# Kernel tuning notes

Hardware: AMD Instinct MI355X
Metric: run time of the kernel (lower is better)

## Reference

```python
import jax, jax.numpy as jnp
import numpy as np

NUM_HEADS = 12

def setup_inputs() -> dict:
    key = jax.random.key(0)
    k1, k2, k3, k4 = jax.random.split(key, 4)
    B, N, D = 8, 1024, 768
    x = jax.random.normal(k1, (B, N, D), dtype=jnp.float32)
    mask = jax.random.randint(k2, (B, N), 0, 2, dtype=jnp.int32)
    Wqkv = jax.random.normal(k3, (3 * D, D), dtype=jnp.float32) * (D ** -0.5)
    Wproj = jax.random.normal(k4, (D, D), dtype=jnp.float32) * (D ** -0.5)
    bproj = jnp.zeros((D,), dtype=jnp.float32)
    return {"x": x, "mask": mask, "Wqkv": Wqkv, "Wproj": Wproj, "bproj": bproj}

def reference(x, mask, Wqkv, Wproj, bproj):
    B, N, D = x.shape
    H = NUM_HEADS
    hd = D // H
    scale = hd ** -0.5
    # QKV projection (no bias), split into q,k,v of shape [B,H,N,hd]
    qkv = jnp.einsum('bnd,ed->bne', x, Wqkv).reshape(B, N, 3, H, hd)
    qkv = jnp.transpose(qkv, (2, 0, 3, 1, 4))
    q, k, v = qkv[0], qkv[1], qkv[2]
    # padding mask: attend where both query and key are valid; masked-out
    # (padded) query rows attend only to themselves (diagonal) to avoid NaNs
    m = mask.astype(bool)  # [B,N]
    pair = m[:, None, :, None] & m[:, None, None, :]          # [B,1,N,N]
    diag = jnp.eye(N, dtype=bool)[None, None]                 # [1,1,N,N]
    attn_mask = pair | (diag & ~m[:, None, :, None])          # [B,1,N,N]
    scores = jnp.einsum('bhnd,bhmd->bhnm', q, k) * scale      # [B,H,N,N]
    scores = jnp.where(attn_mask, scores, jnp.finfo(scores.dtype).min)
    attn = jax.nn.softmax(scores, axis=-1)
    out = jnp.einsum('bhnm,bhmd->bhnd', attn, v)
    out = jnp.transpose(out, (0, 2, 1, 3)).reshape(B, N, D)
    out = jnp.einsum('bnd,ed->bne', out, Wproj) + bproj
    return out
```

## Files before the change

### kernel.cpp

```cpp
#include <hip/hip_runtime.h>
#include <hip/hip_bf16.h>
#include <stdint.h>


typedef unsigned short u16;
typedef unsigned int u32;
typedef __attribute__((ext_vector_type(8))) short short8;
typedef __attribute__((ext_vector_type(4))) float f32x4;

#define MFMA16(a, b, c) __builtin_amdgcn_mfma_f32_16x16x32_bf16((a), (b), (c), 0, 0, 0)

static __device__ __forceinline__ u16 f2bf(float f) {
    __hip_bfloat16 h = __float2bfloat16(f);
    return *(u16*)&h;
}
static __device__ __forceinline__ void gld16(const u16* g, u16* l) {
  __builtin_amdgcn_global_load_lds(
      (const __attribute__((address_space(1))) void*)g,
      (__attribute__((address_space(3))) void*)l, 16, 0, 0);
}

__global__ __launch_bounds__(256) void cvt_bf16(
    const float* __restrict__ s0, u16* __restrict__ d0, int n0,
    const float* __restrict__ s1, u16* __restrict__ d1, int n1,
    const float* __restrict__ s2, u16* __restrict__ d2, int n2) {
  int i = (blockIdx.x * 256 + threadIdx.x) * 4;
  const float* s; u16* d;
  if (i < n0) { s = s0 + i; d = d0 + i; }
  else if ((i -= n0) < n1) { s = s1 + i; d = d1 + i; }
  else if ((i -= n1) < n2) { s = s2 + i; d = d2 + i; }
  else return;
  float4 v = *(const float4*)s;
  ushort4 o;
  o.x = f2bf(v.x); o.y = f2bf(v.y); o.z = f2bf(v.z); o.w = f2bf(v.w);
  *(ushort4*)d = o;
}

__global__ __launch_bounds__(512, 4) void gemm_qkv_p32(
    const u16* __restrict__ A,
    const u16* __restrict__ B,
    u16* __restrict__ C) {
  constexpr int K = 768, LDC = 2304, NTIL = K / 32;
  __shared__ u16 lds[2][(256 + 128) * 32];
  const int tid = threadIdx.x;
  const int w = tid >> 6, l = tid & 63;
  const int lane16 = l & 15, quad = l >> 4;
  const int wr = w >> 2, wc = w & 3;

  const int orig = blockIdx.x;
  const int logical = (orig & 7) * 72 + (orig >> 3);
  const int i0 = (logical / 18) * 256, j0 = (logical % 18) * 128;

  f32x4 acc[8][2];
  #pragma unroll
  for (int m = 0; m < 8; m++)
    #pragma unroll
    for (int n = 0; n < 2; n++) acc[m][n] = (f32x4){0.f, 0.f, 0.f, 0.f};

  auto stage = [&](int buf, int t) {
    const int k0 = t * 32;
    u16* Ad = &lds[buf][0];
    #pragma unroll
    for (int s = 0; s < 2; s++) {
      int lin = tid + s * 512;
      int row = lin >> 2, j = lin & 3;
      gld16(&A[(size_t)(i0 + row) * K + k0 + ((j ^ ((row >> 1) & 3)) * 8)], &Ad[lin * 8]);
    }
    {
      u16* Bd = &lds[buf][256 * 32];
      int row = tid >> 2, j = tid & 3;
      gld16(&B[(size_t)(j0 + row) * K + k0 + ((j ^ ((row >> 1) & 3)) * 8)], &Bd[tid * 8]);
    }
  };

  stage(0, 0);
  stage(1, 1);
  asm volatile("s_waitcnt vmcnt(3)" ::: "memory");
  __builtin_amdgcn_s_barrier();

  for (int t = 0; t < NTIL; t++) {
    const u16* Al = &lds[t & 1][0];
    const u16* Bl = &lds[t & 1][256 * 32];
    short8 bf[2], af[8];
    #pragma unroll
    for (int n = 0; n < 2; n++) {
      int row = wc * 32 + n * 16 + lane16;
      int ch = quad ^ ((row >> 1) & 3);
      bf[n] = *(const short8*)&Bl[row * 32 + ch * 8];
    }
    #pragma unroll
    for (int mi = 0; mi < 8; mi++) {
      int row = wr * 128 + mi * 16 + lane16;
      int ch = quad ^ ((row >> 1) & 3);
      af[mi] = *(const short8*)&Al[row * 32 + ch * 8];
    }
    asm volatile("s_waitcnt lgkmcnt(0)" ::: "memory");
    __builtin_amdgcn_sched_barrier(0);
    __builtin_amdgcn_s_barrier();
    if (t + 2 < NTIL) stage(t & 1, t + 2);
    __builtin_amdgcn_s_setprio(1);
    #pragma unroll
    for (int mi = 0; mi < 8; mi++)
      #pragma unroll
      for (int n = 0; n < 2; n++)
        acc[mi][n] = MFMA16(af[mi], bf[n], acc[mi][n]);
    __builtin_amdgcn_s_setprio(0);
    if (t + 2 < NTIL) asm volatile("s_waitcnt vmcnt(3)" ::: "memory");
    else              asm volatile("s_waitcnt vmcnt(0)" ::: "memory");
    __builtin_amdgcn_s_barrier();
  }

  #pragma unroll
  for (int m = 0; m < 8; m++) {
    #pragma unroll
    for (int n = 0; n < 2; n++) {
      int col = j0 + wc * 32 + n * 16 + lane16;
      #pragma unroll
      for (int r = 0; r < 4; r++) {
        int row = i0 + wr * 128 + m * 16 + quad * 4 + r;
        C[(size_t)row * LDC + col] = f2bf(acc[m][n][r]);
      }
    }
  }
}

__global__ __launch_bounds__(256, 3) void gemm_proj_p32(
    const u16* __restrict__ A,
    const u16* __restrict__ B,
    float* __restrict__ C,
    const float* __restrict__ bias) {
  constexpr int K = 768, LDC = 768, NTIL = K / 32;
  __shared__ u16 lds[2][(128 + 64) * 32];
  const int tid = threadIdx.x;
  const int w = tid >> 6, l = tid & 63;
  const int lane16 = l & 15, quad = l >> 4;
  const int mh = (w & 1) * 64;
  const int nh = (w >> 1) * 32;

  const int orig = blockIdx.x;
  const int logical = (orig & 7) * 96 + (orig >> 3);
  const int i0 = (logical / 12) * 128, j0 = (logical % 12) * 64;

  f32x4 acc[4][2];
  #pragma unroll
  for (int m = 0; m < 4; m++)
    #pragma unroll
    for (int n = 0; n < 2; n++) acc[m][n] = (f32x4){0.f, 0.f, 0.f, 0.f};

  auto stage = [&](int buf, int t) {
    const int k0 = t * 32;
    u16* Ad = &lds[buf][0];
    #pragma unroll
    for (int s = 0; s < 2; s++) {
      int lin = tid + s * 256;
      int row = lin >> 2, j = lin & 3;
      gld16(&A[(size_t)(i0 + row) * K + k0 + ((j ^ ((row >> 1) & 3)) * 8)], &Ad[lin * 8]);
    }
    {
      u16* Bd = &lds[buf][128 * 32];
      int row = tid >> 2, j = tid & 3;
      gld16(&B[(size_t)(j0 + row) * K + k0 + ((j ^ ((row >> 1) & 3)) * 8)], &Bd[tid * 8]);
    }
  };

  stage(0, 0);
  stage(1, 1);
  asm volatile("s_waitcnt vmcnt(3)" ::: "memory");
  __builtin_amdgcn_s_barrier();

  for (int t = 0; t < NTIL; t++) {
    const u16* Al = &lds[t & 1][0];
    const u16* Bl = &lds[t & 1][128 * 32];
    short8 bf[2];
    #pragma unroll
    for (int n = 0; n < 2; n++) {
      int row = nh + n * 16 + lane16;
      int ch = quad ^ ((row >> 1) & 3);
      bf[n] = *(const short8*)&Bl[row * 32 + ch * 8];
    }
    #pragma unroll
    for (int p = 0; p < 2; p++) {
      short8 af[2];
      #pragma unroll
      for (int mi = 0; mi < 2; mi++) {
        int row = mh + (2 * p + mi) * 16 + lane16;
        int ch = quad ^ ((row >> 1) & 3);
        af[mi] = *(const short8*)&Al[row * 32 + ch * 8];
      }
      if (p == 1) {
        asm volatile("s_waitcnt lgkmcnt(0)" ::: "memory");
        __builtin_amdgcn_sched_barrier(0);
        __builtin_amdgcn_s_barrier();
        if (t + 2 < NTIL) stage(t & 1, t + 2);
      }
      __builtin_amdgcn_s_setprio(1);
      #pragma unroll
      for (int mi = 0; mi < 2; mi++)
        #pragma unroll
        for (int n = 0; n < 2; n++)
          acc[2 * p + mi][n] = MFMA16(af[mi], bf[n], acc[2 * p + mi][n]);
      __builtin_amdgcn_s_setprio(0);
    }
    if (t + 2 < NTIL) asm volatile("s_waitcnt vmcnt(3)" ::: "memory");
    else              asm volatile("s_waitcnt vmcnt(0)" ::: "memory");
    __builtin_amdgcn_s_barrier();
  }

  #pragma unroll
  for (int m = 0; m < 4; m++) {
    #pragma unroll
    for (int n = 0; n < 2; n++) {
      int col = j0 + nh + n * 16 + lane16;
      #pragma unroll
      for (int r = 0; r < 4; r++) {
        int row = i0 + mh + m * 16 + quad * 4 + r;
        C[(size_t)row * LDC + col] = acc[m][n][r] + bias[col];
      }
    }
  }
}

__global__ __launch_bounds__(256, 3) void attn_mfma(
    const u16* __restrict__ qkv,
    const int* __restrict__ mask,
    u16* __restrict__ ctx) {
  __shared__ u16 Ks[64][72];
  __shared__ u16 Vt[64][72];
  __shared__ u16 Ps[4][32][72];
  __shared__ float mkb_all[1024];

  const int tid = threadIdx.x;
  const int w = tid >> 6, l = tid & 63;
  const int lane16 = l & 15, quad = l >> 4;
  const int idx = blockIdx.x;
  const int bh = idx % 96;
  const int rb = idx / 96;
  const int b = bh / 12, h = bh % 12;
  const int n0 = rb * 128;
  const int baseRow = b * 1024;

  const float K1 = 0.18033688011112043f;
  const float K0 = -23.083120654223415f;

  const int key_s = tid >> 2, ds_s = (tid & 3) * 16;
  const int kA_s = (tid & 31) * 2, dg_s = tid >> 5;

  {
    int4 mv = *(const int4*)&mask[baseRow + tid * 4];
    f32x4 mf;
    mf[0] = mv.x ? K0 : -1e38f;
    mf[1] = mv.y ? K0 : -1e38f;
    mf[2] = mv.z ? K0 : -1e38f;
    mf[3] = mv.w ? K0 : -1e38f;
    *(f32x4*)&mkb_all[tid * 4] = mf;
  }

  short8 qfrag[2][2];
  #pragma unroll
  for (int qt = 0; qt < 2; qt++) {
    const u16* qp = qkv + (size_t)(baseRow + n0 + w*32 + qt*16 + lane16) * 2304 + h*64;
    #pragma unroll
    for (int ks = 0; ks < 2; ks++)
      qfrag[qt][ks] = *(const short8*)(qp + ks*32 + quad*8);
  }

  f32x4 oacc[2][4];
  #pragma unroll
  for (int qt = 0; qt < 2; qt++)
    #pragma unroll
    for (int nt = 0; nt < 4; nt++) oacc[qt][nt] = (f32x4){0.f, 0.f, 0.f, 0.f};
  f32x4 lsum4[2] = {(f32x4){0.f,0.f,0.f,0.f}, (f32x4){0.f,0.f,0.f,0.f}};

  uint4 kr0, kr1, vr0, vr1;
  {
    const u16* kp = qkv + (size_t)(baseRow + key_s) * 2304 + 768 + h*64 + ds_s;
    kr0 = *(const uint4*)kp;
    kr1 = *(const uint4*)(kp + 8);
    const u16* vp = qkv + (size_t)(baseRow + kA_s) * 2304 + 1536 + h*64 + dg_s*8;
    vr0 = *(const uint4*)vp;
    vr1 = *(const uint4*)(vp + 2304);
  }

  for (int c = 0; c < 16; c++) {
    if (c) __syncthreads();

    *(uint4*)&Ks[key_s][ds_s]     = kr0;
    *(uint4*)&Ks[key_s][ds_s + 8] = kr1;
    {
      const u16* va = (const u16*)&vr0;
      const u16* vb = (const u16*)&vr1;
      #pragma unroll
      for (int j = 0; j < 8; j++)
        *(unsigned int*)&Vt[dg_s*8 + j][kA_s] =
            (unsigned int)va[j] | ((unsigned int)vb[j] << 16);
    }

    if (c + 1 < 16) {
      const u16* kp = qkv + (size_t)(baseRow + (c+1)*64 + key_s) * 2304 + 768 + h*64 + ds_s;
      kr0 = *(const uint4*)kp;
      kr1 = *(const uint4*)(kp + 8);
      const u16* vp = qkv + (size_t)(baseRow + (c+1)*64 + kA_s) * 2304 + 1536 + h*64 + dg_s*8;
      vr0 = *(const uint4*)vp;
      vr1 = *(const uint4*)(vp + 2304);
    }
    __syncthreads();

    f32x4 sacc[4][2];
    #pragma unroll
    for (int kt = 0; kt < 4; kt++)
      #pragma unroll
      for (int qt = 0; qt < 2; qt++) sacc[kt][qt] = (f32x4){0.f, 0.f, 0.f, 0.f};
    #pragma unroll
    for (int ks = 0; ks < 2; ks++) {
      short8 kf[4];
      #pragma unroll
      for (int kt = 0; kt < 4; kt++)
        kf[kt] = *(const short8*)&Ks[kt*16 + lane16][ks*32 + quad*8];
      __builtin_amdgcn_s_setprio(1);
      #pragma unroll
      for (int kt = 0; kt < 4; kt++)
        #pragma unroll
        for (int qt = 0; qt < 2; qt++)
          sacc[kt][qt] = MFMA16(kf[kt], qfrag[qt][ks], sacc[kt][qt]);
      __builtin_amdgcn_s_setprio(0);
    }

    #pragma unroll
    for (int kt = 0; kt < 4; kt++) {
      f32x4 mk4 = *(const f32x4*)&mkb_all[c*64 + kt*16 + quad*4];
      #pragma unroll
      for (int qt = 0; qt < 2; qt++) {
        float e0 = __builtin_amdgcn_exp2f(fmaf(sacc[kt][qt][0], K1, mk4[0]));
        float e1 = __builtin_amdgcn_exp2f(fmaf(sacc[kt][qt][1], K1, mk4[1]));
        float e2 = __builtin_amdgcn_exp2f(fmaf(sacc[kt][qt][2], K1, mk4[2]));
        float e3 = __builtin_amdgcn_exp2f(fmaf(sacc[kt][qt][3], K1, mk4[3]));
        lsum4[qt][0] += e0; lsum4[qt][1] += e1;
        lsum4[qt][2] += e2; lsum4[qt][3] += e3;
        uint2 pv;
        asm("v_cvt_pk_bf16_f32 %0, %1, %2" : "=v"(pv.x) : "v"(e0), "v"(e1));
        asm("v_cvt_pk_bf16_f32 %0, %1, %2" : "=v"(pv.y) : "v"(e2), "v"(e3));
        *(uint2*)&Ps[w][qt*16 + lane16][kt*16 + quad*4] = pv;
      }
    }

    #pragma unroll
    for (int kc = 0; kc < 2; kc++) {
      short8 pf[2], vf[4];
      #pragma unroll
      for (int qt = 0; qt < 2; qt++)
        pf[qt] = *(const short8*)&Ps[w][qt*16 + lane16][kc*32 + quad*8];
      #pragma unroll
      for (int nt = 0; nt < 4; nt++)
        vf[nt] = *(const short8*)&Vt[nt*16 + lane16][kc*32 + quad*8];
      __builtin_amdgcn_s_setprio(1);
      #pragma unroll
      for (int qt = 0; qt < 2; qt++)
        #pragma unroll
        for (int nt = 0; nt < 4; nt++)
          oacc[qt][nt] = MFMA16(pf[qt], vf[nt], oacc[qt][nt]);
      __builtin_amdgcn_s_setprio(0);
    }
  }

  float linv[2][4];
  #pragma unroll
  for (int qt = 0; qt < 2; qt++) {
    float s = lsum4[qt][0] + lsum4[qt][1] + lsum4[qt][2] + lsum4[qt][3];
    s += __shfl_xor(s, 16);
    s += __shfl_xor(s, 32);
    #pragma unroll
    for (int r = 0; r < 4; r++)
      linv[qt][r] = 1.0f / __shfl(s, quad*4 + r);
  }
  #pragma unroll
  for (int qt = 0; qt < 2; qt++) {
    #pragma unroll
    for (int r = 0; r < 4; r++) {
      int rl = w*32 + qt*16 + quad*4 + r;
      int rg = n0 + rl;
      int mq = (mkb_all[n0 + rl] != -1e38f);
      #pragma unroll
      for (int nt = 0; nt < 4; nt++) {
        u16 outv;
        if (mq) {
          outv = f2bf(oacc[qt][nt][r] * linv[qt][r]);
        } else {
          outv = qkv[(size_t)(baseRow + rg) * 2304 + 1536 + h*64 + nt*16 + lane16];
        }
        ctx[(size_t)(baseRow + rg) * 768 + h*64 + nt*16 + lane16] = outv;
      }
    }
  }
}

extern "C" void kernel_launch(void* const* d_in, const int* in_sizes, int n_in,
                              void* d_out, int out_size, void* d_ws, size_t ws_size,
                              hipStream_t stream) {
  const float* x     = (const float*)d_in[0];
  const int*   mask  = (const int*)d_in[1];
  const float* Wqkv  = (const float*)d_in[2];
  const float* Wproj = (const float*)d_in[3];
  const float* bproj = (const float*)d_in[4];
  float* out = (float*)d_out;

  const int NX = 8192 * 768;
  const int NQ = 2304 * 768;
  const int NP = 768 * 768;

  char* wsb = (char*)d_ws;
  u16* qkv    = (u16*)wsb;
  u16* ctx    = (u16*)(wsb + (size_t)8192 * 2304 * 2);
  u16* xb     = (u16*)(wsb + (size_t)8192 * 2304 * 2 + (size_t)8192 * 768 * 2);
  u16* wqkvb  = xb + NX;
  u16* wprojb = wqkvb + NQ;

  int cvt_blocks = ((NX + NQ + NP) / 4 + 255) / 256;
  cvt_bf16<<<dim3(cvt_blocks), 256, 0, stream>>>(x, xb, NX, Wqkv, wqkvb, NQ, Wproj, wprojb, NP);

  gemm_qkv_p32<<<dim3(576), 512, 0, stream>>>(xb, wqkvb, qkv);
  attn_mfma<<<dim3(768), 256, 0, stream>>>(qkv, mask, ctx);
  gemm_proj_p32<<<dim3(768), 256, 0, stream>>>(ctx, wprojb, out, bproj);
}
```

Measured before the change: 183.5 us.

## Double-buffer K/V LDS tiles and apply XOR swizzle instead of padding

Replaces the padded LDS arrays for K, transposed V and P with unpadded 64-column arrays that use an XOR swizzle on 8-element chunks, to avoid bank conflicts on the MFMA fragment reads and writes. K and V tiles become double-buffered by chunk parity, which removes the barrier at the top of each iteration and lets the next tile's stores overlap the previous tile's reads. LDS use grows for K/V but shrinks for padding, so occupancy at 3 blocks per CU may shift. The narrow 4-byte V transposed stores may still conflict.

```diff
diff --git a/kernel.cpp b/kernel.cpp
--- a/kernel.cpp
+++ b/kernel.cpp
@@ -224,9 +224,9 @@
     const u16* __restrict__ qkv,
     const int* __restrict__ mask,
     u16* __restrict__ ctx) {
-  __shared__ u16 Ks[64][72];
-  __shared__ u16 Vt[64][72];
-  __shared__ u16 Ps[4][32][72];
+  __shared__ u16 Ks[2][64][64];
+  __shared__ u16 Vt[2][64][64];
+  __shared__ u16 Ps[4][32][64];
   __shared__ float mkb_all[1024];
 
   const int tid = threadIdx.x;
@@ -282,19 +282,25 @@
   }
 
   for (int c = 0; c < 16; c++) {
-    if (c) __syncthreads();
-
-    *(uint4*)&Ks[key_s][ds_s]     = kr0;
-    *(uint4*)&Ks[key_s][ds_s + 8] = kr1;
+    const int buf = c & 1;
+    {
+      int ch0 = ds_s >> 3;
+      int sw = key_s & 7;
+      *(uint4*)&Ks[buf][key_s][((ch0 ^ sw) << 3)]       = kr0;
+      *(uint4*)&Ks[buf][key_s][(((ch0 + 1) ^ sw) << 3)] = kr1;
+    }
     {
       const u16* va = (const u16*)&vr0;
       const u16* vb = (const u16*)&vr1;
-      #pragma unroll
-      for (int j = 0; j < 8; j++)
-        *(unsigned int*)&Vt[dg_s*8 + j][kA_s] =
-            (unsigned int)va[j] | ((unsigned int)vb[j] << 16);
-    }
-
+      int chv = (tid & 31) >> 2;
+      int off = kA_s & 7;
+      #pragma unroll
+      for (int j = 0; j < 8; j++) {
+        int row = dg_s * 8 + j;
+        *(u32*)&Vt[buf][row][((chv ^ (row & 7)) << 3) + off] =
+            (u32)va[j] | ((u32)vb[j] << 16);
+      }
+    }
     if (c + 1 < 16) {
       const u16* kp = qkv + (size_t)(baseRow + (c+1)*64 + key_s) * 2304 + 768 + h*64 + ds_s;
       kr0 = *(const uint4*)kp;
@@ -314,8 +320,11 @@
     for (int ks = 0; ks < 2; ks++) {
       short8 kf[4];
       #pragma unroll
-      for (int kt = 0; kt < 4; kt++)
-        kf[kt] = *(const short8*)&Ks[kt*16 + lane16][ks*32 + quad*8];
+      for (int kt = 0; kt < 4; kt++) {
+        int row = kt*16 + lane16;
+        int ch = (4*ks + quad) ^ (row & 7);
+        kf[kt] = *(const short8*)&Ks[buf][row][ch << 3];
+      }
       __builtin_amdgcn_s_setprio(1);
       #pragma unroll
       for (int kt = 0; kt < 4; kt++)
@@ -339,7 +348,9 @@
         uint2 pv;
         asm("v_cvt_pk_bf16_f32 %0, %1, %2" : "=v"(pv.x) : "v"(e0), "v"(e1));
         asm("v_cvt_pk_bf16_f32 %0, %1, %2" : "=v"(pv.y) : "v"(e2), "v"(e3));
-        *(uint2*)&Ps[w][qt*16 + lane16][kt*16 + quad*4] = pv;
+        int prow = qt*16 + lane16;
+        int pch = (2*kt + (quad >> 1)) ^ (prow & 7);
+        *(uint2*)&Ps[w][prow][(pch << 3) + (quad & 1) * 4] = pv;
       }
     }
 
@@ -347,11 +358,17 @@
     for (int kc = 0; kc < 2; kc++) {
       short8 pf[2], vf[4];
       #pragma unroll
-      for (int qt = 0; qt < 2; qt++)
-        pf[qt] = *(const short8*)&Ps[w][qt*16 + lane16][kc*32 + quad*8];
-      #pragma unroll
-      for (int nt = 0; nt < 4; nt++)
-        vf[nt] = *(const short8*)&Vt[nt*16 + lane16][kc*32 + quad*8];
+      for (int qt = 0; qt < 2; qt++) {
+        int row = qt*16 + lane16;
+        int ch = (4*kc + quad) ^ (row & 7);
+        pf[qt] = *(const short8*)&Ps[w][row][ch << 3];
+      }
+      #pragma unroll
+      for (int nt = 0; nt < 4; nt++) {
+        int row = nt*16 + lane16;
+        int ch = (4*kc + quad) ^ (row & 7);
+        vf[nt] = *(const short8*)&Vt[buf][row][ch << 3];
+      }
       __builtin_amdgcn_s_setprio(1);
       #pragma unroll
       for (int qt = 0; qt < 2; qt++)
```

New measurement: 187.4 us. 1.02x slower.
